# Kernel optimization log

Measured on AMD Instinct MI355X. Metric: run time of the kernel, lower is better.

## Reference

```python
import jax, jax.numpy as jnp
import numpy as np

NUM_EXPERTS = 8
HIDDEN = 2048
INTER = 1408
N_TOKENS = 8192


def setup_inputs() -> dict:
    key = jax.random.key(0)
    k1, k2, k3, k4, k5 = jax.random.split(key, 5)
    tokens = jax.random.normal(k1, (N_TOKENS, HIDDEN), dtype=jnp.float32)
    local_ids = jax.random.randint(k2, (N_TOKENS,), 0, NUM_EXPERTS)
    weights = jax.random.uniform(k3, (N_TOKENS,), dtype=jnp.float32)
    # kaiming_uniform-ish init scale
    bound1 = 1.0 / np.sqrt(HIDDEN)
    bound2 = 1.0 / np.sqrt(INTER)
    gate_up_proj = jax.random.uniform(k4, (NUM_EXPERTS, 2 * INTER, HIDDEN), dtype=jnp.float32, minval=-bound1, maxval=bound1)
    down_proj = jax.random.uniform(k5, (NUM_EXPERTS, HIDDEN, INTER), dtype=jnp.float32, minval=-bound2, maxval=bound2)
    return {"tokens": tokens, "local_ids": local_ids, "weights": weights,
            "gate_up_proj": gate_up_proj, "down_proj": down_proj}


def reference(tokens, local_ids, weights, gate_up_proj, down_proj):
    # tokens: [N, D]; local_ids: [N]; weights: [N]
    # gate_up_proj: [E, 2I, D]; down_proj: [E, D, I]
    E = gate_up_proj.shape[0]
    out = jnp.zeros_like(tokens)
    for e in range(E):  # fixed small expert loop; masked dense GEMMs
        fc1 = tokens @ gate_up_proj[e].T              # [N, 2I]
        gate, up = jnp.split(fc1, 2, axis=-1)         # SwiGLU convention: first half is gate
        h = jax.nn.silu(gate) * up                    # fused SiLU*up
        h = h * weights[:, None]                      # routing weight before down_proj
        o = h @ down_proj[e].T                        # [N, D]
        out = out + jnp.where((local_ids == e)[:, None], o, 0.0)
    return out
```

## Files before the change

### kernel.cpp

```cpp
#include <hip/hip_runtime.h>
#include <stdint.h>

#define E_    8
#define D_    2048
#define I_    1408
#define TWOI_ 2816
#define N_    8192
#define BM    128
#define MAXTILES 72
#define MPAD  9216

typedef __bf16 bf16x8 __attribute__((ext_vector_type(8)));
typedef float  floatx4 __attribute__((ext_vector_type(4)));

#define M_CNT   0
#define M_CUR   8
#define M_PB    16
#define M_NT    24
#define M_RTE   32
#define M_RTR   104
#define M_RTV   176

#define OFF_PERM  4096ULL
#define OFF_WPAD  40960ULL
#define OFF_APAD  81920ULL
#define OFF_HPAD  37830656ULL
#define OFF_GU    63782912ULL
#define OFF_DN    156057600ULL
#define WS_NEED   202194944ULL

__device__ inline void gload16(const void* g, void* lds) {
  __builtin_amdgcn_global_load_lds(
      (__attribute__((address_space(1))) void*)g,
      (__attribute__((address_space(3))) void*)lds, 16, 0, 0);
}

__device__ inline unsigned short f2bf(float f) {
  unsigned int u = __builtin_bit_cast(unsigned int, f);
  u += 0x7fffu + ((u >> 16) & 1u);
  return (unsigned short)(u >> 16);
}

__global__ void k_hist(const int* __restrict__ ids, int* meta) {
  int i = blockIdx.x * 256 + threadIdx.x;
  int e = ids[i];
  int lane = threadIdx.x & 63;
  for (int ex = 0; ex < E_; ++ex) {
    unsigned long long m = __ballot(e == ex);
    if (lane == 0 && m) atomicAdd(&meta[M_CNT + ex], __popcll(m));
  }
}

__global__ void k_meta(int* meta) {
  if (threadIdx.x != 0) return;
  int padr = 0, tiles = 0;
  for (int e = 0; e < E_; ++e) {
    meta[M_PB + e] = padr;
    int c = meta[M_CNT + e];
    int nt = (c + BM - 1) / BM;
    for (int t = 0; t < nt; ++t) {
      meta[M_RTE + tiles] = e;
      meta[M_RTR + tiles] = padr + t * BM;
      int v = c - t * BM; if (v > BM) v = BM;
      meta[M_RTV + tiles] = v;
      tiles++;
    }
    padr += nt * BM;
  }
  meta[M_NT] = tiles;
}

__global__ void k_scatter(const int* __restrict__ ids, const float* __restrict__ w,
                          int* meta, int* perm, float* wpad) {
  int i = blockIdx.x * 256 + threadIdx.x;
  int e = ids[i];
  float wv = w[i];
  int lane = threadIdx.x & 63;
  for (int ex = 0; ex < E_; ++ex) {
    unsigned long long m = __ballot(e == ex);
    if (!m) continue;
    int base = 0;
    if (lane == 0) base = atomicAdd(&meta[M_CUR + ex], __popcll(m));
    base = __shfl(base, 0);
    if (e == ex) {
      int r = meta[M_PB + ex] + base + __popcll(m & ((1ULL << lane) - 1ULL));
      perm[r] = i;
      wpad[r] = wv;
    }
  }
}

__global__ void k_gather(const float* __restrict__ tokens, const int* __restrict__ perm,
                         unsigned short* __restrict__ apad) {
  int r = blockIdx.x;
  int t = perm[r];
  if (t < 0) return;
  const float4* src = (const float4*)(tokens + (size_t)t * D_);
  uint4* dst = (uint4*)(apad + (size_t)r * D_);
  int i = threadIdx.x;
  float4 a = src[i * 2], b = src[i * 2 + 1];
  union { unsigned short s[8]; uint4 v; } pk;
  pk.s[0] = f2bf(a.x); pk.s[1] = f2bf(a.y); pk.s[2] = f2bf(a.z); pk.s[3] = f2bf(a.w);
  pk.s[4] = f2bf(b.x); pk.s[5] = f2bf(b.y); pk.s[6] = f2bf(b.z); pk.s[7] = f2bf(b.w);
  dst[i] = pk.v;
}

__global__ void k_cvt(const float* __restrict__ src, unsigned short* __restrict__ dst, int n8) {
  int i = blockIdx.x * 256 + threadIdx.x;
  if (i >= n8) return;
  const float4* s4 = (const float4*)src;
  float4 a = s4[i * 2], b = s4[i * 2 + 1];
  union { unsigned short s[8]; uint4 v; } pk;
  pk.s[0] = f2bf(a.x); pk.s[1] = f2bf(a.y); pk.s[2] = f2bf(a.z); pk.s[3] = f2bf(a.w);
  pk.s[4] = f2bf(b.x); pk.s[5] = f2bf(b.y); pk.s[6] = f2bf(b.z); pk.s[7] = f2bf(b.w);
  ((uint4*)dst)[i] = pk.v;
}

__global__ __launch_bounds__(256) void k_gemm1(
    const unsigned short* __restrict__ apad,
    const unsigned short* __restrict__ gub,
    const float* __restrict__ wpad,
    const int* __restrict__ meta,
    unsigned short* __restrict__ hpad) {
  int bid = blockIdx.x;
  int panel = bid / 176;
  int rem = bid - panel * 176;
  int ct = rem >> 3;
  int rt = panel * 8 + (rem & 7);
  if (rt >= meta[M_NT]) return;
  int e = meta[M_RTE + rt], row0 = meta[M_RTR + rt], nv = meta[M_RTV + rt];

  __shared__ __attribute__((aligned(16))) __bf16 As[2][BM * 32];
  __shared__ __attribute__((aligned(16))) __bf16 Bgs[2][64 * 32];
  __shared__ __attribute__((aligned(16))) __bf16 Bus[2][64 * 32];

  int tid = threadIdx.x;
  int lane = tid & 63;
  int wave = __builtin_amdgcn_readfirstlane(tid >> 6);

  const __bf16* A  = (const __bf16*)apad + (size_t)row0 * D_;
  const __bf16* Bg = (const __bf16*)gub + ((size_t)e * TWOI_ + (size_t)ct * 64) * D_;
  const __bf16* Bu = Bg + (size_t)I_ * D_;

  int srow = lane >> 2;
  int skq  = (lane & 3) * 8;

  floatx4 zero = {0.f, 0.f, 0.f, 0.f};
  floatx4 accg[2][4], accu[2][4];
#pragma unroll
  for (int mi = 0; mi < 2; ++mi)
#pragma unroll
    for (int ni = 0; ni < 4; ++ni) { accg[mi][ni] = zero; accu[mi][ni] = zero; }

  int quad8 = (lane >> 4) * 8;
  int l16 = lane & 15;

  for (int k0 = 0; k0 < D_; k0 += 64) {
#pragma unroll
    for (int p = 0; p < 2; ++p) {
      int kk = k0 + p * 32;
      gload16(A + (size_t)(wave * 16 + srow) * D_ + kk + skq, &As[p][(wave * 16) * 32]);
      gload16(A + (size_t)(64 + wave * 16 + srow) * D_ + kk + skq, &As[p][(64 + wave * 16) * 32]);
      gload16(Bg + (size_t)(wave * 16 + srow) * D_ + kk + skq, &Bgs[p][(wave * 16) * 32]);
      gload16(Bu + (size_t)(wave * 16 + srow) * D_ + kk + skq, &Bus[p][(wave * 16) * 32]);
    }
    __syncthreads();
#pragma unroll
    for (int p = 0; p < 2; ++p) {
      bf16x8 af[2], bg[4], bu[4];
#pragma unroll
      for (int mi = 0; mi < 2; ++mi)
        af[mi] = *(const bf16x8*)&As[p][(wave * 32 + mi * 16 + l16) * 32 + quad8];
#pragma unroll
      for (int ni = 0; ni < 4; ++ni) {
        bg[ni] = *(const bf16x8*)&Bgs[p][(ni * 16 + l16) * 32 + quad8];
        bu[ni] = *(const bf16x8*)&Bus[p][(ni * 16 + l16) * 32 + quad8];
      }
#pragma unroll
      for (int mi = 0; mi < 2; ++mi)
#pragma unroll
        for (int ni = 0; ni < 4; ++ni) {
          accg[mi][ni] = __builtin_amdgcn_mfma_f32_16x16x32_bf16(af[mi], bg[ni], accg[mi][ni], 0, 0, 0);
          accu[mi][ni] = __builtin_amdgcn_mfma_f32_16x16x32_bf16(af[mi], bu[ni], accu[mi][ni], 0, 0, 0);
        }
    }
    __syncthreads();
  }

  int quad = lane >> 4;
#pragma unroll
  for (int mi = 0; mi < 2; ++mi)
#pragma unroll
    for (int reg = 0; reg < 4; ++reg) {
      int r = wave * 32 + mi * 16 + quad * 4 + reg;
      if (r < nv) {
        float wgt = wpad[row0 + r];
        unsigned short* hrow = hpad + (size_t)(row0 + r) * I_ + (size_t)ct * 64;
#pragma unroll
        for (int ni = 0; ni < 4; ++ni) {
          float g = accg[mi][ni][reg];
          float u = accu[mi][ni][reg];
          float s = g / (1.f + __expf(-g));
          hrow[ni * 16 + l16] = f2bf(s * u * wgt);
        }
      }
    }
}

__global__ __launch_bounds__(256) void k_gemm2(
    const unsigned short* __restrict__ hpad,
    const unsigned short* __restrict__ dnb,
    const int* __restrict__ meta,
    const int* __restrict__ perm,
    float* __restrict__ out) {
  int bid = blockIdx.x;
  int panel = bid / 128;
  int rem = bid - panel * 128;
  int ct = rem >> 3;
  int rt = panel * 8 + (rem & 7);
  if (rt >= meta[M_NT]) return;
  int e = meta[M_RTE + rt], row0 = meta[M_RTR + rt], nv = meta[M_RTV + rt];

  __shared__ __attribute__((aligned(16))) __bf16 As[2][128 * 32];
  __shared__ __attribute__((aligned(16))) __bf16 Bs[2][128 * 32];

  int tid = threadIdx.x;
  int lane = tid & 63;
  int wave = __builtin_amdgcn_readfirstlane(tid >> 6);
  int wm = wave >> 1, wn = wave & 1;

  const __bf16* A = (const __bf16*)hpad + (size_t)row0 * I_;
  const __bf16* B = (const __bf16*)dnb + ((size_t)e * D_ + (size_t)ct * 128) * I_;

  int srow = lane >> 2;
  int skq = (lane & 3) * 8;

  floatx4 zero = {0.f, 0.f, 0.f, 0.f};
  floatx4 acc[4][4];
#pragma unroll
  for (int mi = 0; mi < 4; ++mi)
#pragma unroll
    for (int ni = 0; ni < 4; ++ni) acc[mi][ni] = zero;

  int quad8 = (lane >> 4) * 8;
  int l16 = lane & 15;

  for (int k0 = 0; k0 < I_; k0 += 64) {
#pragma unroll
    for (int p = 0; p < 2; ++p) {
      int kk = k0 + p * 32;
      gload16(A + (size_t)(wave * 16 + srow) * I_ + kk + skq, &As[p][(wave * 16) * 32]);
      gload16(A + (size_t)(64 + wave * 16 + srow) * I_ + kk + skq, &As[p][(64 + wave * 16) * 32]);
      gload16(B + (size_t)(wave * 16 + srow) * I_ + kk + skq, &Bs[p][(wave * 16) * 32]);
      gload16(B + (size_t)(64 + wave * 16 + srow) * I_ + kk + skq, &Bs[p][(64 + wave * 16) * 32]);
    }
    __syncthreads();
#pragma unroll
    for (int p = 0; p < 2; ++p) {
      bf16x8 af[4], bfr[4];
#pragma unroll
      for (int mi = 0; mi < 4; ++mi)
        af[mi] = *(const bf16x8*)&As[p][(wm * 64 + mi * 16 + l16) * 32 + quad8];
#pragma unroll
      for (int ni = 0; ni < 4; ++ni)
        bfr[ni] = *(const bf16x8*)&Bs[p][(wn * 64 + ni * 16 + l16) * 32 + quad8];
#pragma unroll
      for (int mi = 0; mi < 4; ++mi)
#pragma unroll
        for (int ni = 0; ni < 4; ++ni)
          acc[mi][ni] = __builtin_amdgcn_mfma_f32_16x16x32_bf16(af[mi], bfr[ni], acc[mi][ni], 0, 0, 0);
    }
    __syncthreads();
  }

  int quad = lane >> 4;
#pragma unroll
  for (int mi = 0; mi < 4; ++mi)
#pragma unroll
    for (int reg = 0; reg < 4; ++reg) {
      int r = wm * 64 + mi * 16 + quad * 4 + reg;
      if (r < nv) {
        int t = perm[row0 + r];
        float* orow = out + (size_t)t * D_ + (size_t)ct * 128 + wn * 64;
#pragma unroll
        for (int ni = 0; ni < 4; ++ni)
          orow[ni * 16 + l16] = acc[mi][ni][reg];
      }
    }
}

__global__ __launch_bounds__(256) void k_naive(
    const float* __restrict__ tokens, const int* __restrict__ ids,
    const float* __restrict__ w, const float* __restrict__ gu,
    const float* __restrict__ dn, float* __restrict__ out) {
  __shared__ float tok[D_];
  __shared__ float h[I_];
  int t = blockIdx.x;
  int e = ids[t];
  float wgt = w[t];
  for (int i = threadIdx.x; i < D_; i += 256) tok[i] = tokens[(size_t)t * D_ + i];
  __syncthreads();
  for (int j = threadIdx.x; j < I_; j += 256) {
    const float* wg = gu + ((size_t)e * TWOI_ + j) * D_;
    const float* wu = wg + (size_t)I_ * D_;
    float g = 0.f, u = 0.f;
    for (int k = 0; k < D_; ++k) { g += tok[k] * wg[k]; u += tok[k] * wu[k]; }
    h[j] = g / (1.f + __expf(-g)) * u * wgt;
  }
  __syncthreads();
  for (int d = threadIdx.x; d < D_; d += 256) {
    const float* wd = dn + ((size_t)e * D_ + d) * I_;
    float acc = 0.f;
    for (int k = 0; k < I_; ++k) acc += h[k] * wd[k];
    out[(size_t)t * D_ + d] = acc;
  }
}

extern "C" void kernel_launch(void* const* d_in, const int* in_sizes, int n_in,
                              void* d_out, int out_size, void* d_ws, size_t ws_size,
                              hipStream_t stream) {
  const float* tokens = (const float*)d_in[0];
  const int*   ids    = (const int*)d_in[1];
  const float* wts    = (const float*)d_in[2];
  const float* gu     = (const float*)d_in[3];
  const float* dn     = (const float*)d_in[4];
  float* out = (float*)d_out;

  if (ws_size < (size_t)WS_NEED) {
    k_naive<<<N_, 256, 0, stream>>>(tokens, ids, wts, gu, dn, out);
    return;
  }

  char* ws = (char*)d_ws;
  int* meta = (int*)ws;
  int* perm = (int*)(ws + OFF_PERM);
  float* wpad = (float*)(ws + OFF_WPAD);
  unsigned short* apad = (unsigned short*)(ws + OFF_APAD);
  unsigned short* hpad = (unsigned short*)(ws + OFF_HPAD);
  unsigned short* gub  = (unsigned short*)(ws + OFF_GU);
  unsigned short* dnb  = (unsigned short*)(ws + OFF_DN);

  hipMemsetAsync(meta, 0, 64, stream);
  hipMemsetAsync(perm, 0xFF, MPAD * 4, stream);
  k_hist<<<N_ / 256, 256, 0, stream>>>(ids, meta);
  k_meta<<<1, 1, 0, stream>>>(meta);
  k_scatter<<<N_ / 256, 256, 0, stream>>>(ids, wts, meta, perm, wpad);
  k_gather<<<MPAD, 256, 0, stream>>>(tokens, perm, apad);
  int ngu8 = E_ * TWOI_ * D_ / 8;
  int ndn8 = E_ * D_ * I_ / 8;
  k_cvt<<<(ngu8 + 255) / 256, 256, 0, stream>>>(gu, gub, ngu8);
  k_cvt<<<(ndn8 + 255) / 256, 256, 0, stream>>>(dn, dnb, ndn8);
  k_gemm1<<<9 * 176, 256, 0, stream>>>(apad, gub, wpad, meta, hpad);
  k_gemm2<<<9 * 128, 256, 0, stream>>>(hpad, dnb, meta, perm, out);
}
```

Before: 660.9 us.

## Rewrite gate/up GEMM with 256x128 tiles, swizzled LDS and phased pipelining

The first expert GEMM is rebuilt around 512-thread blocks that each compute a 256-row super-tile against 128 gate and 128 up columns. Operands are double-buffered in XOR-swizzled shared memory, and loads are interleaved with four MFMA phases using explicit vmcnt waits, barriers and setprio. The metadata kernel adds a list of 256-row super-tiles per expert, and block IDs are remapped across 8 groups, likely to spread work across XCDs. The goal is more operand reuse per load, fewer LDS bank conflicts and better overlap of memory with compute. The cost is heavy register pressure and more padded rows in partially filled super-tiles.

```diff
diff --git a/kernel.cpp b/kernel.cpp
--- a/kernel.cpp
+++ b/kernel.cpp
@@ -9,6 +9,8 @@
 #define BM    128
 #define MAXTILES 72
 #define MPAD  9216
+#define MAXST 40
+#define NCT1  11
 
 typedef __bf16 bf16x8 __attribute__((ext_vector_type(8)));
 typedef float  floatx4 __attribute__((ext_vector_type(4)));
@@ -20,6 +22,10 @@
 #define M_RTE   32
 #define M_RTR   104
 #define M_RTV   176
+#define M_NST   248
+#define M_STE   256
+#define M_STR   296
+#define M_STV   336
 
 #define OFF_PERM  4096ULL
 #define OFF_WPAD  40960ULL
@@ -68,6 +74,19 @@
     padr += nt * BM;
   }
   meta[M_NT] = tiles;
+  int nst = 0;
+  for (int e = 0; e < E_; ++e) {
+    int c = meta[M_CNT + e];
+    int pb = meta[M_PB + e];
+    for (int off = 0; off < c; off += 256) {
+      meta[M_STE + nst] = e;
+      meta[M_STR + nst] = pb + off;
+      int v = c - off; if (v > 256) v = 256;
+      meta[M_STV + nst] = v;
+      nst++;
+    }
+  }
+  meta[M_NST] = nst;
 }
 
 __global__ void k_scatter(const int* __restrict__ ids, const float* __restrict__ w,
@@ -116,95 +135,162 @@
   ((uint4*)dst)[i] = pk.v;
 }
 
-__global__ __launch_bounds__(256) void k_gemm1(
+
+#define RD_A(h, s)                                                            \
+  {                                                                           \
+    const char* baseA_ = (const char*)&Abuf[s][h][0];                         \
+    _Pragma("unroll") for (int mf = 0; mf < 4; ++mf) {                        \
+      af[mf][0] = *(const bf16x8*)(baseA_ + rbA + mf * 2048 + swz0);          \
+      af[mf][1] = *(const bf16x8*)(baseA_ + rbA + mf * 2048 + swz1);          \
+    }                                                                         \
+  }
+
+#define RD_B(h, s)                                                            \
+  {                                                                           \
+    const char* baseB_ = (const char*)&Bbuf[s][h][0];                         \
+    _Pragma("unroll") for (int nf = 0; nf < 2; ++nf) {                        \
+      bq[nf][0] = *(const bf16x8*)(baseB_ + cbB + nf * 2048 + swz0);          \
+      bq[nf][1] = *(const bf16x8*)(baseB_ + cbB + nf * 2048 + swz1);          \
+    }                                                                         \
+  }
+
+#define MFMA_PH(qi)                                                           \
+  __builtin_amdgcn_s_setprio(1);                                              \
+  _Pragma("unroll") for (int mf = 0; mf < 4; ++mf) {                          \
+    _Pragma("unroll") for (int nf = 0; nf < 2; ++nf) {                        \
+      acc[qi][mf][nf] = __builtin_amdgcn_mfma_f32_16x16x32_bf16(              \
+          af[mf][0], bq[nf][0], acc[qi][mf][nf], 0, 0, 0);                    \
+      acc[qi][mf][nf] = __builtin_amdgcn_mfma_f32_16x16x32_bf16(              \
+          af[mf][1], bq[nf][1], acc[qi][mf][nf], 0, 0, 0);                    \
+    }                                                                         \
+  }                                                                           \
+  __builtin_amdgcn_s_setprio(0);
+
+#define PH_MID()                                                              \
+  __builtin_amdgcn_sched_barrier(0);                                          \
+  __builtin_amdgcn_s_barrier();                                               \
+  asm volatile("s_waitcnt lgkmcnt(0)" ::: "memory");                          \
+  __builtin_amdgcn_sched_barrier(0);
+
+#define PH_END()    __builtin_amdgcn_s_barrier();
+#define PH_END_V6() asm volatile("s_waitcnt vmcnt(6)" ::: "memory"); \
+                    __builtin_amdgcn_s_barrier();
+#define PH_END_V8() asm volatile("s_waitcnt vmcnt(8)" ::: "memory"); \
+                    __builtin_amdgcn_s_barrier();
+
+#define STAGE(P, BUF, s, h)                                                   \
+  gload16(P, &BUF[s][h][ldst]);                                               \
+  gload16(P + 64 * D_, &BUF[s][h][4096 + ldst]);                              \
+  P += 64;
+
+__global__ __launch_bounds__(512, 2) void k_gemm1(
     const unsigned short* __restrict__ apad,
     const unsigned short* __restrict__ gub,
     const float* __restrict__ wpad,
     const int* __restrict__ meta,
     unsigned short* __restrict__ hpad) {
+  int nst = meta[M_NST];
+  int active = nst * NCT1;
   int bid = blockIdx.x;
-  int panel = bid / 176;
-  int rem = bid - panel * 176;
-  int ct = rem >> 3;
-  int rt = panel * 8 + (rem & 7);
-  if (rt >= meta[M_NT]) return;
-  int e = meta[M_RTE + rt], row0 = meta[M_RTR + rt], nv = meta[M_RTV + rt];
-
-  __shared__ __attribute__((aligned(16))) __bf16 As[2][BM * 32];
-  __shared__ __attribute__((aligned(16))) __bf16 Bgs[2][64 * 32];
-  __shared__ __attribute__((aligned(16))) __bf16 Bus[2][64 * 32];
+  if (bid >= active) return;
+  int x = bid & 7, idx = bid >> 3;
+  int q = active >> 3, r = active & 7;
+  int wgid = (x < r ? x * (q + 1) : r * (q + 1) + (x - r) * q) + idx;
+  int st = wgid / NCT1;
+  int ct = wgid - st * NCT1;
+  int e = meta[M_STE + st], row0 = meta[M_STR + st], nv = meta[M_STV + st];
+
+  __shared__ __attribute__((aligned(16))) __bf16 Abuf[2][2][128 * 64];
+  __shared__ __attribute__((aligned(16))) __bf16 Bbuf[2][2][128 * 64];
 
   int tid = threadIdx.x;
   int lane = tid & 63;
   int wave = __builtin_amdgcn_readfirstlane(tid >> 6);
-
-  const __bf16* A  = (const __bf16*)apad + (size_t)row0 * D_;
-  const __bf16* Bg = (const __bf16*)gub + ((size_t)e * TWOI_ + (size_t)ct * 64) * D_;
-  const __bf16* Bu = Bg + (size_t)I_ * D_;
-
-  int srow = lane >> 2;
-  int skq  = (lane & 3) * 8;
+  int wm = wave >> 2, wn = wave & 3;
+  int l16 = lane & 15, qd = lane >> 4;
+
+  int r0 = tid >> 3;
+  int jl8 = (((tid >> 3) ^ tid) & 7) * 8;
+  const __bf16* pa0 = (const __bf16*)apad + (size_t)(row0 + r0) * D_ + jl8;
+  const __bf16* pa1 = pa0 + (size_t)128 * D_;
+  const __bf16* pb0 = (const __bf16*)gub +
+      ((size_t)e * TWOI_ + (size_t)ct * 128 + r0) * D_ + jl8;
+  const __bf16* pb1 = pb0 + (size_t)I_ * D_;
+  int ldst = wave * 512;
+
+  int swz0 = ((qd ^ (l16 & 7)) & 7) * 16;
+  int swz1 = (((4 + qd) ^ (l16 & 7)) & 7) * 16;
+  int rbA = (wm * 64 + l16) * 128;
+  int cbB = (wn * 32 + l16) * 128;
 
   floatx4 zero = {0.f, 0.f, 0.f, 0.f};
-  floatx4 accg[2][4], accu[2][4];
-#pragma unroll
-  for (int mi = 0; mi < 2; ++mi)
-#pragma unroll
-    for (int ni = 0; ni < 4; ++ni) { accg[mi][ni] = zero; accu[mi][ni] = zero; }
-
-  int quad8 = (lane >> 4) * 8;
-  int l16 = lane & 15;
-
-  for (int k0 = 0; k0 < D_; k0 += 64) {
-#pragma unroll
-    for (int p = 0; p < 2; ++p) {
-      int kk = k0 + p * 32;
-      gload16(A + (size_t)(wave * 16 + srow) * D_ + kk + skq, &As[p][(wave * 16) * 32]);
-      gload16(A + (size_t)(64 + wave * 16 + srow) * D_ + kk + skq, &As[p][(64 + wave * 16) * 32]);
-      gload16(Bg + (size_t)(wave * 16 + srow) * D_ + kk + skq, &Bgs[p][(wave * 16) * 32]);
-      gload16(Bu + (size_t)(wave * 16 + srow) * D_ + kk + skq, &Bus[p][(wave * 16) * 32]);
-    }
-    __syncthreads();
-#pragma unroll
-    for (int p = 0; p < 2; ++p) {
-      bf16x8 af[2], bg[4], bu[4];
-#pragma unroll
-      for (int mi = 0; mi < 2; ++mi)
-        af[mi] = *(const bf16x8*)&As[p][(wave * 32 + mi * 16 + l16) * 32 + quad8];
-#pragma unroll
-      for (int ni = 0; ni < 4; ++ni) {
-        bg[ni] = *(const bf16x8*)&Bgs[p][(ni * 16 + l16) * 32 + quad8];
-        bu[ni] = *(const bf16x8*)&Bus[p][(ni * 16 + l16) * 32 + quad8];
-      }
-#pragma unroll
-      for (int mi = 0; mi < 2; ++mi)
-#pragma unroll
-        for (int ni = 0; ni < 4; ++ni) {
-          accg[mi][ni] = __builtin_amdgcn_mfma_f32_16x16x32_bf16(af[mi], bg[ni], accg[mi][ni], 0, 0, 0);
-          accu[mi][ni] = __builtin_amdgcn_mfma_f32_16x16x32_bf16(af[mi], bu[ni], accu[mi][ni], 0, 0, 0);
-        }
-    }
-    __syncthreads();
-  }
-
-  int quad = lane >> 4;
-#pragma unroll
-  for (int mi = 0; mi < 2; ++mi)
-#pragma unroll
-    for (int reg = 0; reg < 4; ++reg) {
-      int r = wave * 32 + mi * 16 + quad * 4 + reg;
-      if (r < nv) {
-        float wgt = wpad[row0 + r];
-        unsigned short* hrow = hpad + (size_t)(row0 + r) * I_ + (size_t)ct * 64;
-#pragma unroll
-        for (int ni = 0; ni < 4; ++ni) {
-          float g = accg[mi][ni][reg];
-          float u = accu[mi][ni][reg];
-          float s = g / (1.f + __expf(-g));
-          hrow[ni * 16 + l16] = f2bf(s * u * wgt);
+  floatx4 acc[4][4][2];
+#pragma unroll
+  for (int a = 0; a < 4; ++a)
+#pragma unroll
+    for (int b = 0; b < 4; ++b)
+#pragma unroll
+      for (int c = 0; c < 2; ++c) acc[a][b][c] = zero;
+
+  STAGE(pa0, Abuf, 0, 0)
+  STAGE(pb0, Bbuf, 0, 0)
+  STAGE(pa1, Abuf, 0, 1)
+  STAGE(pb1, Bbuf, 0, 1)
+  STAGE(pa0, Abuf, 1, 0)
+  STAGE(pb0, Bbuf, 1, 0)
+  asm volatile("s_waitcnt vmcnt(8)" ::: "memory");
+  __builtin_amdgcn_s_barrier();
+
+  bf16x8 af[4][2], bq[2][2];
+  for (int t = 0; t < 32; t += 2) {
+#pragma unroll
+    for (int u = 0; u < 2; ++u) {
+      int tl = t + u;
+      RD_A(0, u)
+      RD_B(0, u)
+      if (tl + 1 < 32) { STAGE(pa1, Abuf, u ^ 1, 1) }
+      PH_MID()
+      MFMA_PH(0)
+      PH_END_V6()
+      RD_B(1, u)
+      if (tl + 1 < 32) { STAGE(pb1, Bbuf, u ^ 1, 1) }
+      PH_MID()
+      MFMA_PH(1)
+      PH_END()
+      RD_A(1, u)
+      RD_B(0, u)
+      if (tl + 2 < 32) { STAGE(pa0, Abuf, u, 0) }
+      PH_MID()
+      MFMA_PH(2)
+      PH_END()
+      RD_B(1, u)
+      if (tl + 2 < 32) { STAGE(pb0, Bbuf, u, 0) }
+      PH_MID()
+      MFMA_PH(3)
+      PH_END_V8()
+    }
+  }
+
+#pragma unroll
+  for (int mi2 = 0; mi2 < 2; ++mi2)
+#pragma unroll
+    for (int mf = 0; mf < 4; ++mf)
+#pragma unroll
+      for (int reg = 0; reg < 4; ++reg) {
+        int lr = mi2 * 128 + wm * 64 + mf * 16 + qd * 4 + reg;
+        if (lr < nv) {
+          float wgt = wpad[row0 + lr];
+          unsigned short* hrow = hpad + (size_t)(row0 + lr) * I_ +
+                                 (size_t)ct * 128 + wn * 32 + l16;
+#pragma unroll
+          for (int nf = 0; nf < 2; ++nf) {
+            float g = acc[mi2 * 2 + 0][mf][nf][reg];
+            float uu = acc[mi2 * 2 + 1][mf][nf][reg];
+            float s = g / (1.f + __expf(-g));
+            hrow[nf * 16] = f2bf(s * uu * wgt);
+          }
         }
       }
-    }
 }
 
 __global__ __launch_bounds__(256) void k_gemm2(
@@ -350,6 +436,6 @@
   int ndn8 = E_ * D_ * I_ / 8;
   k_cvt<<<(ngu8 + 255) / 256, 256, 0, stream>>>(gu, gub, ngu8);
   k_cvt<<<(ndn8 + 255) / 256, 256, 0, stream>>>(dn, dnb, ndn8);
-  k_gemm1<<<9 * 176, 256, 0, stream>>>(apad, gub, wpad, meta, hpad);
+  k_gemm1<<<NCT1 * MAXST, 512, 0, stream>>>(apad, gub, wpad, meta, hpad);
   k_gemm2<<<9 * 128, 256, 0, stream>>>(hpad, dnb, meta, perm, out);
 }
```

Measured after the change: 662.3 us. About the same (+0.2%).
